# Kernel tuning notes

Hardware: AMD Instinct MI355X
Metric: run time of the kernel (lower is better)

## Reference

```python
import jax, jax.numpy as jnp
import numpy as np

N = 30000      # nodes
E = 480000     # edges (before self-loops)
IN = 32        # input_dim
H = 8          # heads
C = 64         # hidden_dim (per-head out channels)
HC = H * C     # 512, concat width
L = 3          # num_layers
NEG_SLOPE = 0.2  # PyG GATConv default


def setup_inputs() -> dict:
    key = jax.random.key(0)
    ks = jax.random.split(key, 16)
    s = 0.05
    return {
        "x": jax.random.normal(ks[0], (N, IN), jnp.float32),
        "edge_index": jax.random.randint(ks[1], (2, E), 0, N, jnp.int32),
        # input projection
        "W_in": jax.random.normal(ks[2], (IN, HC), jnp.float32) * s,
        "b_in": jnp.zeros((HC,), jnp.float32),
        # stacked GATConv params (L layers)
        "W_gat": jax.random.normal(ks[3], (L, HC, HC), jnp.float32) * s,
        "att_src": jax.random.normal(ks[4], (L, H, C), jnp.float32) * s,
        "att_dst": jax.random.normal(ks[5], (L, H, C), jnp.float32) * s,
        "b_gat": jnp.zeros((L, HC), jnp.float32),
        # heads
        "W_att": jax.random.normal(ks[6], (HC, H), jnp.float32) * s,
        "b_att": jnp.zeros((H,), jnp.float32),
        "W_h1": jax.random.normal(ks[7], (HC, C), jnp.float32) * s,
        "b_h1": jnp.zeros((C,), jnp.float32),
        "W_h2": jax.random.normal(ks[8], (C, 1), jnp.float32) * s,
        "b_h2": jnp.zeros((1,), jnp.float32),
    }


def _gat_layer(h, src, dst, W, a_src, a_dst, b):
    # h: [N, HC]; src/dst: [E'] (with self-loops)
    hp = (h @ W).reshape(N, H, C)                       # per-head features
    s = jnp.einsum('nhc,hc->nh', hp, a_src)             # [N, H]
    d = jnp.einsum('nhc,hc->nh', hp, a_dst)             # [N, H]
    e = jax.nn.leaky_relu(s[src] + d[dst], NEG_SLOPE)   # [E', H]
    # segment softmax over destination neighborhoods
    m = jax.ops.segment_max(e, dst, num_segments=N)     # [N, H]
    ex = jnp.exp(e - m[dst])
    den = jax.ops.segment_sum(ex, dst, num_segments=N)
    alpha = ex / (den[dst] + 1e-16)                     # [E', H]
    msg = hp[src] * alpha[:, :, None]                   # [E', H, C]
    out = jax.ops.segment_sum(msg, dst, num_segments=N).reshape(N, HC) + b
    return out


def reference(x, edge_index, W_in, b_in, W_gat, att_src, att_dst, b_gat,
              W_att, b_att, W_h1, b_h1, W_h2, b_h2):
    # PyG GATConv adds self-loops by default
    loops = jnp.arange(N, dtype=edge_index.dtype)
    src = jnp.concatenate([edge_index[0], loops])
    dst = jnp.concatenate([edge_index[1], loops])

    h = jax.nn.relu(x @ W_in + b_in)                    # input_proj + ReLU
    for l in range(L):
        h = jax.nn.relu(_gat_layer(h, src, dst, W_gat[l], att_src[l], att_dst[l], b_gat[l]))
        # dropout is identity in eval mode
    attention_weights = jax.nn.softmax(h @ W_att + b_att, axis=1)   # [N, H]
    anomaly_scores = jax.nn.sigmoid(jax.nn.relu(h @ W_h1 + b_h1) @ W_h2 + b_h2)  # [N, 1]
    return (anomaly_scores, attention_weights)
```

## Files before the change

### kernel.cpp

```cpp
#include <hip/hip_runtime.h>
#include <hip/hip_bf16.h>
#include <math.h>

#define HCW 512
#define NHD 8
#define CCH 64

typedef unsigned short u16;
typedef unsigned int   u32;
typedef __attribute__((ext_vector_type(8))) short bf16x8;
typedef __attribute__((ext_vector_type(4))) float f32x4;

__device__ __forceinline__ float bf2f(u32 u) {
  union { float f; u32 i; } v; v.i = u << 16; return v.f;
}
__device__ __forceinline__ u16 f2bf(float f) {
  u32 x = __builtin_bit_cast(u32, f);
  return (u16)((x + 0x7fff + ((x >> 16) & 1)) >> 16);
}
__device__ __forceinline__ void gload_lds16(const void* g, void* l) {
  __builtin_amdgcn_global_load_lds(
      (const __attribute__((address_space(1))) u32*)g,
      (__attribute__((address_space(3))) u32*)l, 16, 0, 0);
}

__global__ void k_hist(const int* __restrict__ ei, int* __restrict__ deg, int E, int N) {
  int e = blockIdx.x * blockDim.x + threadIdx.x;
  if (e >= E + N) return;
  int dst = (e < E) ? ei[E + e] : (e - E);
  atomicAdd(&deg[dst], 1);
}

__global__ __launch_bounds__(256) void k_alloc(const int* __restrict__ deg, int* __restrict__ beg,
                                               int* __restrict__ cursor, int N) {
  int n = blockIdx.x * 256 + threadIdx.x;
  int lane = threadIdx.x & 63;
  int v = (n < N) ? deg[n] : 0;
  int incl = v;
  #pragma unroll
  for (int off = 1; off < 64; off <<= 1) {
    int t = __shfl_up(incl, off);
    if (lane >= off) incl += t;
  }
  int total = __shfl(incl, 63);
  int base = 0;
  if (lane == 63) base = atomicAdd(cursor, total);
  base = __shfl(base, 63);
  if (n < N) beg[n] = base + incl - v;
}

__global__ void k_fill(const int* __restrict__ ei, const int* __restrict__ beg,
                       int* __restrict__ cnt, int* __restrict__ csr_src, int E, int N) {
  int e = blockIdx.x * blockDim.x + threadIdx.x;
  if (e >= E + N) return;
  int src, dst;
  if (e < E) { src = ei[e]; dst = ei[E + e]; } else { src = e - E; dst = e - E; }
  int pos = beg[dst] + atomicAdd(&cnt[dst], 1);
  csr_src[pos] = src;
}

__global__ __launch_bounds__(256) void k_prep(const float* __restrict__ W_gat, u16* __restrict__ Wt,
                                              const float* __restrict__ W_h1, const float* __restrict__ W_att,
                                              u16* __restrict__ Wf,
                                              const float* __restrict__ x, u16* __restrict__ xb, int xtotal,
                                              const float* __restrict__ W_in, u16* __restrict__ Wtin,
                                              int XB) {
  __shared__ float sm[32][33];
  int b = blockIdx.x;
  int t = threadIdx.x;
  if (b < 768) {
    int l = b >> 8, rem = b & 255;
    int n0 = (rem & 15) * 32, k0 = (rem >> 4) * 32;
    const float* Wl = W_gat + (size_t)l * HCW * HCW;
    u16* Wtl = Wt + (size_t)l * HCW * HCW;
    int tx = t & 31, ty = t >> 5;
    #pragma unroll
    for (int r = 0; r < 32; r += 8)
      sm[ty + r][tx] = Wl[(size_t)(k0 + ty + r) * HCW + n0 + tx];
    __syncthreads();
    #pragma unroll
    for (int r = 0; r < 32; r += 8)
      Wtl[(size_t)(n0 + ty + r) * HCW + k0 + tx] = f2bf(sm[tx][ty + r]);
  } else if (b < 848) {
    int n = b - 768;
    for (int k = t; k < 512; k += 256) {
      float v = 0.f;
      if (n < 64) v = W_h1[(size_t)k * 64 + n];
      else if (n < 72) v = W_att[(size_t)k * 8 + (n - 64)];
      Wf[(size_t)n * 512 + k] = f2bf(v);
    }
  } else if (b < 848 + XB) {
    int i = ((b - 848) * 256 + t) * 8;
    if (i < xtotal) {
      float4 a = *(const float4*)(x + i);
      float4 bb = *(const float4*)(x + i + 4);
      uint4 o;
      o.x = (u32)f2bf(a.x) | ((u32)f2bf(a.y) << 16);
      o.y = (u32)f2bf(a.z) | ((u32)f2bf(a.w) << 16);
      o.z = (u32)f2bf(bb.x) | ((u32)f2bf(bb.y) << 16);
      o.w = (u32)f2bf(bb.z) | ((u32)f2bf(bb.w) << 16);
      *(uint4*)(xb + i) = o;
    }
  } else {
    int idx = (b - 848 - XB) * 256 + t;
    int n = idx >> 5, k = idx & 31;
    Wtin[idx] = f2bf(W_in[(size_t)k * HCW + n]);
  }
}

__global__ __launch_bounds__(256) void k_inproj3(const u16* __restrict__ xb, const u16* __restrict__ Wt,
                                                 const float* __restrict__ b, u16* __restrict__ h, int N) {
  __shared__ u16 As[128 * 32];
  __shared__ u16 Bs[128 * 32];
  int tid = threadIdx.x, lane = tid & 63, w = tid >> 6;
  int bm = blockIdx.y * 128, bn = blockIdx.x * 128;
  #pragma unroll
  for (int it = 0; it < 4; it++) {
    int g = it * 256 + tid;
    if (g < 512) {
      int row = g >> 2, gb = g & 3, gs = gb ^ (row & 3);
      int ar = bm + row; if (ar >= N) ar = N - 1;
      gload_lds16(xb + (size_t)ar * 32 + gs * 8, &As[g * 8]);
    } else {
      int gg = g - 512;
      int row = gg >> 2, gb = gg & 3, gs = gb ^ (row & 3);
      gload_lds16(Wt + (size_t)(bn + row) * 32 + gs * 8, &Bs[gg * 8]);
    }
  }
  __syncthreads();
  bf16x8 af[2];
  #pragma unroll
  for (int i = 0; i < 2; i++) {
    int rowA = w * 32 + i * 16 + (lane & 15);
    int gA = (lane >> 4) ^ (rowA & 3);
    af[i] = *(const bf16x8*)&As[rowA * 32 + gA * 8];
  }
  f32x4 acc[2][8] = {};
  #pragma unroll
  for (int j = 0; j < 8; j++) {
    int rowB = j * 16 + (lane & 15);
    int gB = (lane >> 4) ^ (rowB & 3);
    bf16x8 bfr = *(const bf16x8*)&Bs[rowB * 32 + gB * 8];
    #pragma unroll
    for (int i = 0; i < 2; i++)
      acc[i][j] = __builtin_amdgcn_mfma_f32_16x16x32_bf16(af[i], bfr, acc[i][j], 0, 0, 0);
  }
  #pragma unroll
  for (int j = 0; j < 8; j++) {
    int col = bn + j * 16 + (lane & 15);
    float bb = b[col];
    #pragma unroll
    for (int i = 0; i < 2; i++) {
      #pragma unroll
      for (int r = 0; r < 4; r++) {
        int n = bm + w * 32 + i * 16 + (lane >> 4) * 4 + r;
        if (n < N) h[(size_t)n * HCW + col] = f2bf(fmaxf(acc[i][j][r] + bb, 0.f));
      }
    }
  }
}

__global__ __launch_bounds__(256) void k_gemm_mfma(const u16* __restrict__ A,
                                                   const u16* __restrict__ Bt,
                                                   u16* __restrict__ C,
                                                   const float* __restrict__ a_src,
                                                   const float* __restrict__ a_dst,
                                                   float* __restrict__ sarr,
                                                   float* __restrict__ darr,
                                                   int M) {
  int nPanels = (M + 127) >> 7;
  int lin = blockIdx.y * 4 + blockIdx.x;
  int xcd = lin & 7;
  int t = lin >> 3;
  int bn_i = t & 3;
  int p = t >> 2;
  int bm_i = p * 8 + xcd;
  if (bm_i >= nPanels) return;
  int bm = bm_i * 128, bn = bn_i * 128;

  __shared__ u16 As[128 * 64];
  __shared__ u16 Bs[128 * 64];
  int tid = threadIdx.x;
  int lane = tid & 63, w = tid >> 6;
  int wr = w >> 1, wc = w & 1;
  f32x4 acc[4][4] = {};
  for (int k0 = 0; k0 < 512; k0 += 64) {
    __syncthreads();
    #pragma unroll
    for (int it = 0; it < 4; it++) {
      int g = it * 256 + tid;
      int row = g >> 3;
      int gb = g & 7;
      int gs = gb ^ (row & 7);
      int ar = bm + row; if (ar >= M) ar = M - 1;
      gload_lds16(A + (size_t)ar * HCW + k0 + gs * 8, &As[g * 8]);
      gload_lds16(Bt + (size_t)(bn + row) * HCW + k0 + gs * 8, &Bs[g * 8]);
    }
    __syncthreads();
    #pragma unroll
    for (int ks = 0; ks < 2; ks++) {
      bf16x8 af[4], bfr[4];
      #pragma unroll
      for (int f = 0; f < 4; f++) {
        int rowA = wr * 64 + f * 16 + (lane & 15);
        int gA = ((ks * 4 + (lane >> 4)) ^ (rowA & 7));
        af[f] = *(const bf16x8*)&As[rowA * 64 + gA * 8];
        int rowB = wc * 64 + f * 16 + (lane & 15);
        int gB = ((ks * 4 + (lane >> 4)) ^ (rowB & 7));
        bfr[f] = *(const bf16x8*)&Bs[rowB * 64 + gB * 8];
      }
      #pragma unroll
      for (int i = 0; i < 4; i++)
        #pragma unroll
        for (int j = 0; j < 4; j++)
          acc[i][j] = __builtin_amdgcn_mfma_f32_16x16x32_bf16(af[i], bfr[j], acc[i][j], 0, 0, 0);
    }
  }
  int gr_base = bm + wr * 64;
  int gc_base = bn + wc * 64;
  #pragma unroll
  for (int i = 0; i < 4; i++) {
    #pragma unroll
    for (int j = 0; j < 4; j++) {
      int col = gc_base + j * 16 + (lane & 15);
      #pragma unroll
      for (int r = 0; r < 4; r++) {
        int rowg = gr_base + i * 16 + (lane >> 4) * 4 + r;
        if (rowg < M) C[(size_t)rowg * HCW + col] = f2bf(acc[i][j][r]);
      }
    }
  }
  int head = (bn >> 6) + wc;
  float asv[4], adv[4];
  #pragma unroll
  for (int j = 0; j < 4; j++) {
    asv[j] = a_src[head * 64 + j * 16 + (lane & 15)];
    adv[j] = a_dst[head * 64 + j * 16 + (lane & 15)];
  }
  #pragma unroll
  for (int i = 0; i < 4; i++) {
    #pragma unroll
    for (int r = 0; r < 4; r++) {
      float sv = acc[i][0][r] * asv[0] + acc[i][1][r] * asv[1]
               + acc[i][2][r] * asv[2] + acc[i][3][r] * asv[3];
      float dv = acc[i][0][r] * adv[0] + acc[i][1][r] * adv[1]
               + acc[i][2][r] * adv[2] + acc[i][3][r] * adv[3];
      sv += __shfl_xor(sv, 1); dv += __shfl_xor(dv, 1);
      sv += __shfl_xor(sv, 2); dv += __shfl_xor(dv, 2);
      sv += __shfl_xor(sv, 4); dv += __shfl_xor(dv, 4);
      sv += __shfl_xor(sv, 8); dv += __shfl_xor(dv, 8);
      if ((lane & 15) == 0) {
        int rowg = gr_base + i * 16 + (lane >> 4) * 4 + r;
        if (rowg < M) {
          sarr[(size_t)rowg * NHD + head] = sv;
          darr[(size_t)rowg * NHD + head] = dv;
        }
      }
    }
  }
}

__global__ __launch_bounds__(256) void k_agg10(const int* __restrict__ beg_, const int* __restrict__ deg_,
                                               const int* __restrict__ csr_src,
                                               const u16* __restrict__ hp, const float* __restrict__ s,
                                               const float* __restrict__ d, const float* __restrict__ bias,
                                               u16* __restrict__ hout, int N) {
  int hd = blockIdx.x;
  int wv = threadIdx.x >> 6, lane = threadIdx.x & 63;
  int nslot = lane >> 3;
  int q = lane & 7;
  int c = hd * 64 + q * 8;
  int n = blockIdx.y * 32 + wv * 8 + nslot;
  if (n >= N) return;
  int beg = beg_[n], end = beg + deg_[n];
  float dn = d[(size_t)n * NHD + hd];
  const u16* hpc = hp + c;
  float acc[8] = {0.f, 0.f, 0.f, 0.f, 0.f, 0.f, 0.f, 0.f};
  float den = 0.f;

  int i = beg;
  for (; i + 2 <= end; i += 2) {
    int s0 = csr_src[i], s1 = csr_src[i + 1];
    float e0 = s[(size_t)s0 * NHD + hd] + dn;
    float e1 = s[(size_t)s1 * NHD + hd] + dn;
    uint4 v0 = *(const uint4*)(hpc + (size_t)s0 * HCW);
    uint4 v1 = *(const uint4*)(hpc + (size_t)s1 * HCW);
    e0 = (e0 > 0.f) ? e0 : 0.2f * e0;
    e1 = (e1 > 0.f) ? e1 : 0.2f * e1;
    float x0 = __expf(e0), x1 = __expf(e1);
    den += x0 + x1;
    u32 w0[4] = {v0.x, v0.y, v0.z, v0.w};
    u32 w1[4] = {v1.x, v1.y, v1.z, v1.w};
    #pragma unroll
    for (int j = 0; j < 4; j++) {
      acc[2 * j]     += x0 * bf2f(w0[j] & 0xffff) + x1 * bf2f(w1[j] & 0xffff);
      acc[2 * j + 1] += x0 * bf2f(w0[j] >> 16)    + x1 * bf2f(w1[j] >> 16);
    }
  }
  if (i < end) {
    int s0 = csr_src[i];
    float e0 = s[(size_t)s0 * NHD + hd] + dn;
    uint4 v0 = *(const uint4*)(hpc + (size_t)s0 * HCW);
    e0 = (e0 > 0.f) ? e0 : 0.2f * e0;
    float x0 = __expf(e0);
    den += x0;
    u32 w0[4] = {v0.x, v0.y, v0.z, v0.w};
    #pragma unroll
    for (int j = 0; j < 4; j++) {
      acc[2 * j]     += x0 * bf2f(w0[j] & 0xffff);
      acc[2 * j + 1] += x0 * bf2f(w0[j] >> 16);
    }
  }

  float inv = 1.f / (den + 1e-16f);
  float4 bv0 = *(const float4*)(bias + c);
  float4 bv1 = *(const float4*)(bias + c + 4);
  float bb[8] = {bv0.x, bv0.y, bv0.z, bv0.w, bv1.x, bv1.y, bv1.z, bv1.w};
  u32 out[4];
  #pragma unroll
  for (int j = 0; j < 4; j++) {
    float o0 = fmaxf(acc[2 * j] * inv + bb[2 * j], 0.f);
    float o1 = fmaxf(acc[2 * j + 1] * inv + bb[2 * j + 1], 0.f);
    out[j] = (u32)f2bf(o0) | ((u32)f2bf(o1) << 16);
  }
  *(uint4*)(hout + (size_t)n * HCW + c) = make_uint4(out[0], out[1], out[2], out[3]);
}

__global__ __launch_bounds__(256) void k_final2(const u16* __restrict__ A,
                                                const u16* __restrict__ Wf,
                                                const float* __restrict__ b_att,
                                                const float* __restrict__ b_h1,
                                                const float* __restrict__ W_h2,
                                                const float* __restrict__ b_h2,
                                                float* __restrict__ anomaly, float* __restrict__ attw,
                                                int M) {
  __shared__ u16 As[128 * 64];
  __shared__ u16 Bs[80 * 64];
  __shared__ float so[4][32][84];
  int tid = threadIdx.x;
  int lane = tid & 63, w = tid >> 6;
  int bm = blockIdx.x * 128;
  f32x4 acc[2][5] = {};
  for (int k0 = 0; k0 < 512; k0 += 64) {
    __syncthreads();
    #pragma unroll
    for (int it = 0; it < 7; it++) {
      int g = it * 256 + tid;
      if (g < 1024) {
        int row = g >> 3, gb = g & 7;
        int gs = gb ^ (row & 7);
        int ar = bm + row; if (ar >= M) ar = M - 1;
        gload_lds16(A + (size_t)ar * HCW + k0 + gs * 8, &As[g * 8]);
      } else if (g < 1664) {
        int gg = g - 1024;
        int row = gg >> 3, gb = gg & 7;
        int gs = gb ^ (row & 7);
        gload_lds16(Wf + (size_t)row * 512 + k0 + gs * 8, &Bs[gg * 8]);
      }
    }
    __syncthreads();
    #pragma unroll
    for (int ks = 0; ks < 2; ks++) {
      bf16x8 af[2], bfr[5];
      #pragma unroll
      for (int i = 0; i < 2; i++) {
        int rowA = w * 32 + i * 16 + (lane & 15);
        int gA = ((ks * 4 + (lane >> 4)) ^ (rowA & 7));
        af[i] = *(const bf16x8*)&As[rowA * 64 + gA * 8];
      }
      #pragma unroll
      for (int j = 0; j < 5; j++) {
        int rowB = j * 16 + (lane & 15);
        int gB = ((ks * 4 + (lane >> 4)) ^ (rowB & 7));
        bfr[j] = *(const bf16x8*)&Bs[rowB * 64 + gB * 8];
      }
      #pragma unroll
      for (int i = 0; i < 2; i++)
        #pragma unroll
        for (int j = 0; j < 5; j++)
          acc[i][j] = __builtin_amdgcn_mfma_f32_16x16x32_bf16(af[i], bfr[j], acc[i][j], 0, 0, 0);
    }
  }
  #pragma unroll
  for (int i = 0; i < 2; i++) {
    #pragma unroll
    for (int j = 0; j < 5; j++) {
      int col = j * 16 + (lane & 15);
      #pragma unroll
      for (int r = 0; r < 4; r++) {
        int row_l = i * 16 + (lane >> 4) * 4 + r;
        so[w][row_l][col] = acc[i][j][r];
      }
    }
  }
  int row_l = lane >> 1, half = lane & 1;
  int n = bm + w * 32 + row_l;
  if (n < M) {
    float hacc = 0.f;
    #pragma unroll
    for (int kk = 0; kk < 32; kk++) {
      int cc = half * 32 + kk;
      float v = fmaxf(so[w][row_l][cc] + b_h1[cc], 0.f);
      hacc += v * W_h2[cc];
    }
    hacc += __shfl_xor(hacc, 1);
    if (half == 0) {
      anomaly[n] = 1.f / (1.f + __expf(-(hacc + b_h2[0])));
    } else {
      float lg[8];
      float mx = -1e30f;
      #pragma unroll
      for (int j = 0; j < 8; j++) {
        lg[j] = so[w][row_l][64 + j] + b_att[j];
        mx = fmaxf(mx, lg[j]);
      }
      float sum = 0.f;
      #pragma unroll
      for (int j = 0; j < 8; j++) { lg[j] = __expf(lg[j] - mx); sum += lg[j]; }
      float inv = 1.f / sum;
      #pragma unroll
      for (int j = 0; j < 8; j++) attw[(size_t)n * 8 + j] = lg[j] * inv;
    }
  }
}

extern "C" void kernel_launch(void* const* d_in, const int* in_sizes, int n_in,
                              void* d_out, int out_size, void* d_ws, size_t ws_size,
                              hipStream_t stream) {
  const float* x       = (const float*)d_in[0];
  const int*   ei      = (const int*)d_in[1];
  const float* W_in    = (const float*)d_in[2];
  const float* b_in    = (const float*)d_in[3];
  const float* W_gat   = (const float*)d_in[4];
  const float* att_src = (const float*)d_in[5];
  const float* att_dst = (const float*)d_in[6];
  const float* b_gat   = (const float*)d_in[7];
  const float* W_att   = (const float*)d_in[8];
  const float* b_att   = (const float*)d_in[9];
  const float* W_h1    = (const float*)d_in[10];
  const float* b_h1    = (const float*)d_in[11];
  const float* W_h2    = (const float*)d_in[12];
  const float* b_h2    = (const float*)d_in[13];

  const int N  = in_sizes[0] / 32;
  const int E  = in_sizes[1] / 2;
  const int ET = E + N;

  char* ws = (char*)d_ws;
  size_t off = 0;
  auto alloc = [&](size_t bytes) -> void* {
    void* p = ws + off;
    off = (off + bytes + 255) & ~(size_t)255;
    return p;
  };
  u16* h     = (u16*)alloc((size_t)N * HCW * 2);
  u16* hp    = (u16*)alloc((size_t)N * HCW * 2);
  u16* Wt    = (u16*)alloc((size_t)3 * HCW * HCW * 2);
  u16* Wf    = (u16*)alloc((size_t)80 * 512 * 2);
  u16* xb    = (u16*)alloc((size_t)N * 32 * 2);
  u16* Wtin  = (u16*)alloc((size_t)512 * 32 * 2);
  float* sarr = (float*)alloc((size_t)N * NHD * 4);
  float* darr = (float*)alloc((size_t)N * NHD * 4);
  int* zbuf   = (int*)alloc((size_t)(2 * N + 64) * 4);
  int* deg    = zbuf;
  int* cnt    = zbuf + N;
  int* cursor = zbuf + 2 * N;
  int* beg    = (int*)alloc((size_t)N * 4);
  int* csr    = (int*)alloc((size_t)ET * 4);

  float* anomaly = (float*)d_out;
  float* attw    = (float*)d_out + N;

  hipMemsetAsync(zbuf, 0, (size_t)(2 * N + 1) * 4, stream);

  int gbE = (ET + 255) / 256;
  int nb  = (N + 255) / 256;
  k_hist<<<gbE, 256, 0, stream>>>(ei, deg, E, N);
  k_alloc<<<nb, 256, 0, stream>>>(deg, beg, cursor, N);
  k_fill<<<gbE, 256, 0, stream>>>(ei, beg, cnt, csr, E, N);

  int xtotal = N * 32;
  int XB = (xtotal / 8 + 255) / 256;
  k_prep<<<848 + XB + 64, 256, 0, stream>>>(W_gat, Wt, W_h1, W_att, Wf, x, xb, xtotal,
                                            W_in, Wtin, XB);
  k_inproj3<<<dim3(4, (N + 127) / 128), 256, 0, stream>>>(xb, Wtin, b_in, h, N);

  int nPanels = (N + 127) / 128;
  int nPanelsPad = ((nPanels + 7) / 8) * 8;
  dim3 ggrid(4, nPanelsPad);
  dim3 agrid(8, (N + 31) / 32);
  for (int l = 0; l < 3; l++) {
    k_gemm_mfma<<<ggrid, 256, 0, stream>>>(h, Wt + (size_t)l * HCW * HCW, hp,
                                           att_src + (size_t)l * NHD * CCH,
                                           att_dst + (size_t)l * NHD * CCH,
                                           sarr, darr, N);
    k_agg10<<<agrid, 256, 0, stream>>>(beg, deg, csr, hp, sarr, darr,
                                       b_gat + (size_t)l * HCW, h, N);
  }

  k_final2<<<(N + 127) / 128, 256, 0, stream>>>(h, Wf, b_att, b_h1, W_h2, b_h2,
                                                anomaly, attw, N);
}
```

Measured before the change: 414.7 us.

## Sort destination nodes by degree to balance aggregation work across warps

Adds a degree-histogram counting sort (bin counts in k_alloc, prefix scan, scatter into a permutation) so the aggregation kernel processes nodes grouped by similar in-degree. This aims to cut intra-wavefront divergence, since the 8 nodes sharing a wavefront now have similar neighbor-loop trip counts. In exchange it adds two small kernels and an extra indirection per node, and output writes become scattered rather than contiguous across neighboring node slots.

Result: slower. 597.7 us (+44.1%).

```diff
diff --git a/kernel.cpp b/kernel.cpp
--- a/kernel.cpp
+++ b/kernel.cpp
@@ -32,7 +32,7 @@
 }
 
 __global__ __launch_bounds__(256) void k_alloc(const int* __restrict__ deg, int* __restrict__ beg,
-                                               int* __restrict__ cursor, int N) {
+                                               int* __restrict__ cursor, int* __restrict__ dbin, int N) {
   int n = blockIdx.x * 256 + threadIdx.x;
   int lane = threadIdx.x & 63;
   int v = (n < N) ? deg[n] : 0;
@@ -46,7 +46,10 @@
   int base = 0;
   if (lane == 63) base = atomicAdd(cursor, total);
   base = __shfl(base, 63);
-  if (n < N) beg[n] = base + incl - v;
+  if (n < N) {
+    beg[n] = base + incl - v;
+    atomicAdd(&dbin[v < 63 ? v : 63], 1);
+  }
 }
 
 __global__ void k_fill(const int* __restrict__ ei, const int* __restrict__ beg,
@@ -57,6 +60,27 @@
   if (e < E) { src = ei[e]; dst = ei[E + e]; } else { src = e - E; dst = e - E; }
   int pos = beg[dst] + atomicAdd(&cnt[dst], 1);
   csr_src[pos] = src;
+}
+
+__global__ __launch_bounds__(64) void k_dpre(const int* __restrict__ dbin, int* __restrict__ dbase) {
+  int lane = threadIdx.x;
+  int v = dbin[lane];
+  int incl = v;
+  #pragma unroll
+  for (int off = 1; off < 64; off <<= 1) {
+    int t = __shfl_up(incl, off);
+    if (lane >= off) incl += t;
+  }
+  dbase[lane] = incl - v;
+}
+
+__global__ __launch_bounds__(256) void k_dscat(const int* __restrict__ deg, const int* __restrict__ dbase,
+                                               int* __restrict__ dcnt, int* __restrict__ perm, int N) {
+  int n = blockIdx.x * 256 + threadIdx.x;
+  if (n >= N) return;
+  int b = deg[n]; b = (b < 63) ? b : 63;
+  int pos = dbase[b] + atomicAdd(&dcnt[b], 1);
+  perm[pos] = n;
 }
 
 __global__ __launch_bounds__(256) void k_prep(const float* __restrict__ W_gat, u16* __restrict__ Wt,
@@ -260,7 +284,8 @@
   }
 }
 
-__global__ __launch_bounds__(256) void k_agg10(const int* __restrict__ beg_, const int* __restrict__ deg_,
+__global__ __launch_bounds__(256) void k_agg11(const int* __restrict__ perm,
+                                               const int* __restrict__ beg_, const int* __restrict__ deg_,
                                                const int* __restrict__ csr_src,
                                                const u16* __restrict__ hp, const float* __restrict__ s,
                                                const float* __restrict__ d, const float* __restrict__ bias,
@@ -270,8 +295,9 @@
   int nslot = lane >> 3;
   int q = lane & 7;
   int c = hd * 64 + q * 8;
-  int n = blockIdx.y * 32 + wv * 8 + nslot;
-  if (n >= N) return;
+  int gid = blockIdx.y * 32 + wv * 8 + nslot;
+  if (gid >= N) return;
+  int n = perm[gid];
   int beg = beg_[n], end = beg + deg_[n];
   float dn = d[(size_t)n * NHD + hd];
   const u16* hpc = hp + c;
@@ -461,23 +487,29 @@
   u16* Wtin  = (u16*)alloc((size_t)512 * 32 * 2);
   float* sarr = (float*)alloc((size_t)N * NHD * 4);
   float* darr = (float*)alloc((size_t)N * NHD * 4);
-  int* zbuf   = (int*)alloc((size_t)(2 * N + 64) * 4);
+  int* zbuf   = (int*)alloc((size_t)(2 * N + 256) * 4);
   int* deg    = zbuf;
   int* cnt    = zbuf + N;
   int* cursor = zbuf + 2 * N;
+  int* dbin   = zbuf + 2 * N + 64;
+  int* dcnt   = zbuf + 2 * N + 128;
   int* beg    = (int*)alloc((size_t)N * 4);
+  int* dbase  = (int*)alloc((size_t)64 * 4);
+  int* perm   = (int*)alloc((size_t)N * 4);
   int* csr    = (int*)alloc((size_t)ET * 4);
 
   float* anomaly = (float*)d_out;
   float* attw    = (float*)d_out + N;
 
-  hipMemsetAsync(zbuf, 0, (size_t)(2 * N + 1) * 4, stream);
+  hipMemsetAsync(zbuf, 0, (size_t)(2 * N + 192) * 4, stream);
 
   int gbE = (ET + 255) / 256;
   int nb  = (N + 255) / 256;
   k_hist<<<gbE, 256, 0, stream>>>(ei, deg, E, N);
-  k_alloc<<<nb, 256, 0, stream>>>(deg, beg, cursor, N);
+  k_alloc<<<nb, 256, 0, stream>>>(deg, beg, cursor, dbin, N);
   k_fill<<<gbE, 256, 0, stream>>>(ei, beg, cnt, csr, E, N);
+  k_dpre<<<1, 64, 0, stream>>>(dbin, dbase);
+  k_dscat<<<nb, 256, 0, stream>>>(deg, dbase, dcnt, perm, N);
 
   int xtotal = N * 32;
   int XB = (xtotal / 8 + 255) / 256;
@@ -494,7 +526,7 @@
                                            att_src + (size_t)l * NHD * CCH,
                                            att_dst + (size_t)l * NHD * CCH,
                                            sarr, darr, N);
-    k_agg10<<<agrid, 256, 0, stream>>>(beg, deg, csr, hp, sarr, darr,
+    k_agg11<<<agrid, 256, 0, stream>>>(perm, beg, deg, csr, hp, sarr, darr,
                                        b_gat + (size_t)l * HCW, h, N);
   }
 
```
